# Kernel tuning notes

Hardware: AMD Instinct MI355X
Metric: run time of the kernel (lower is better)

## Reference

```python
import jax, jax.numpy as jnp
import numpy as np

D = 1024
H = 16
DH = D // H  # 64


def setup_inputs() -> dict:
    key = jax.random.key(0)
    ks = jax.random.split(key, 7)
    X = jax.random.normal(ks[0], (2, 2048, D), dtype=jnp.float32)
    # Per-head projection weights stacked along head axis: [H, D, DH]
    s = 1.0 / np.sqrt(D)
    Wq = jax.random.uniform(ks[1], (H, D, DH), jnp.float32, -s, s)
    Wk = jax.random.uniform(ks[2], (H, D, DH), jnp.float32, -s, s)
    Wv = jax.random.uniform(ks[3], (H, D, DH), jnp.float32, -s, s)
    bq = jax.random.uniform(ks[4], (H, DH), jnp.float32, -s, s)
    bk = jax.random.uniform(ks[5], (H, DH), jnp.float32, -s, s)
    bv = jax.random.uniform(ks[6], (H, DH), jnp.float32, -s, s)
    return {"X": X, "Wq": Wq, "bq": bq, "Wk": Wk, "bk": bk, "Wv": Wv, "bv": bv}


def reference(X, Wq, bq, Wk, bk, Wv, bv):
    B, S, _ = X.shape
    # Per-head linear projections (batched over heads): [B, H, S, DH]
    Q = jnp.einsum('bsd,hde->bhse', X, Wq) + bq[None, :, None, :]
    K = jnp.einsum('bsd,hde->bhse', X, Wk) + bk[None, :, None, :]
    V = jnp.einsum('bsd,hde->bhse', X, Wv) + bv[None, :, None, :]
    scale = jnp.sqrt(jnp.asarray(DH, dtype=X.dtype))
    QK = jnp.einsum('bhse,bhte->bhst', Q, K) / scale  # [B, H, S, S]
    # Faithful to source: softmax over full row FIRST, then lower-tri mask
    # (post-softmax tril, no renormalization).
    sQK = jax.nn.softmax(QK, axis=-1)
    tril = jnp.tril(jnp.ones((S, S), dtype=X.dtype))
    sQK = sQK * tril
    out = jnp.einsum('bhst,bhte->bhse', sQK, V)  # [B, H, S, DH]
    # Concatenate heads along feature dim (torch.cat over per-head outputs)
    return out.transpose(0, 2, 1, 3).reshape(B, S, H * DH)
```

## Files before the change

### kernel.cpp

```cpp
#include <hip/hip_runtime.h>
#include <math.h>

#define B_  2
#define S_  2048
#define D_  1024
#define H_  16
#define DH_ 64

typedef unsigned short u16;
typedef unsigned int   u32;
typedef _Float16       f16;
typedef _Float16 half8  __attribute__((ext_vector_type(8)));
typedef _Float16 half4  __attribute__((ext_vector_type(4)));
typedef float    f32x4  __attribute__((ext_vector_type(4)));

#if __has_builtin(__builtin_amdgcn_exp2f)
#define EXP2(x) __builtin_amdgcn_exp2f(x)
#else
#define EXP2(x) exp2f(x)
#endif

__device__ __forceinline__ u16 h_bits(f16 h){ return __builtin_bit_cast(u16, h); }

__device__ __forceinline__ void split8(float4 a, float4 b, uint4& H, uint4& L){
    float fv[8] = {a.x, a.y, a.z, a.w, b.x, b.y, b.z, b.w};
    u32 hw[4], lw[4];
    #pragma unroll
    for (int j = 0; j < 4; ++j){
        f16 h0 = (f16)fv[2*j],   h1 = (f16)fv[2*j+1];
        f16 l0 = (f16)(fv[2*j]   - (float)h0);
        f16 l1 = (f16)(fv[2*j+1] - (float)h1);
        hw[j] = h_bits(h0) | ((u32)h_bits(h1) << 16);
        lw[j] = h_bits(l0) | ((u32)h_bits(l1) << 16);
    }
    H = (uint4){hw[0], hw[1], hw[2], hw[3]};
    L = (uint4){lw[0], lw[1], lw[2], lw[3]};
}

__global__ __launch_bounds__(256) void prep_kernel(
    const float* __restrict__ Wq, const float* __restrict__ Wk,
    const float* __restrict__ Wv, u16* __restrict__ Wt)
{
    __shared__ float Wf[64][65];
    const int wb = blockIdx.x;
    const int c  = threadIdx.x;
    const int d0 = (wb & 15) * 64;
    const int h  = (wb >> 4) & 15;
    const int which = wb >> 8;
    const float* src = (which == 0) ? Wq : (which == 1) ? Wk : Wv;
    src += (size_t)h * D_ * DH_;

    #pragma unroll
    for (int it = 0; it < 4; ++it){
        int d  = (c >> 4) + 16 * it;
        int e4 = (c & 15) * 4;
        float4 v = *(const float4*)(src + (size_t)(d0 + d) * DH_ + e4);
        Wf[d][e4+0] = v.x; Wf[d][e4+1] = v.y; Wf[d][e4+2] = v.z; Wf[d][e4+3] = v.w;
    }
    __syncthreads();
    u16* dst = Wt + (size_t)(which * H_ + h) * DH_ * D_;
    #pragma unroll
    for (int it = 0; it < 4; ++it){
        int e  = (c >> 4) + 16 * it;
        int d4 = (c & 15) * 4;
        u16 q[4];
        #pragma unroll
        for (int j = 0; j < 4; ++j)
            q[j] = h_bits((f16)(Wf[d4 + j][e] * 64.0f));
        u32* p = (u32*)(dst + (size_t)e * D_ + d0 + d4);
        p[0] = q[0] | ((u32)q[1] << 16);
        p[1] = q[2] | ((u32)q[3] << 16);
    }
}

#define PKS 40

__global__ __launch_bounds__(256, 3) void proj_kernel(
    const float* __restrict__ X,
    const u16* __restrict__ Wt,
    const float* __restrict__ bq, const float* __restrict__ bk,
    const float* __restrict__ bv,
    f16* __restrict__ Qh, f16* __restrict__ Kh, f16* __restrict__ Vt)
{
    __shared__ u16 XsHi[128 * PKS], XsLo[128 * PKS], Bs[128 * PKS];

    const int tid  = threadIdx.x;
    const int lane = tid & 63;
    const int w    = tid >> 6;
    const int quad = lane >> 4;
    const int ln   = lane & 15;
    const int wr   = (w >> 1) * 64;
    const int wc   = (w & 1) * 64;
    const int m0   = blockIdx.x * 128;
    const int c0   = blockIdx.y * 128;

    const int sr  = tid >> 2;
    const int sch = (tid & 3) * 8;

    const float* x0 = X + (size_t)(m0 + sr) * D_ + sch;
    const float* x1 = x0 + (size_t)64 * D_;
    const u16*  wb0 = Wt + (size_t)(c0 + sr) * D_ + sch;
    const u16*  wb1 = wb0 + (size_t)64 * D_;

    float4 p00 = *(const float4*)x0, p01 = *(const float4*)(x0 + 4);
    float4 p10 = *(const float4*)x1, p11 = *(const float4*)(x1 + 4);
    uint4 rw0 = *(const uint4*)wb0, rw1 = *(const uint4*)wb1;
    uint4 h0, l0, h1, l1;
    split8(p00, p01, h0, l0);
    split8(p10, p11, h1, l1);

    f32x4 acc[4][4];
    #pragma unroll
    for (int i = 0; i < 4; ++i)
        #pragma unroll
        for (int j = 0; j < 4; ++j)
            acc[i][j] = (f32x4){0.f, 0.f, 0.f, 0.f};

    for (int k0 = 0; k0 < D_; k0 += 32){
        __syncthreads();
        *(uint4*)&XsHi[sr * PKS + sch]        = h0;
        *(uint4*)&XsHi[(sr + 64) * PKS + sch] = h1;
        *(uint4*)&XsLo[sr * PKS + sch]        = l0;
        *(uint4*)&XsLo[(sr + 64) * PKS + sch] = l1;
        *(uint4*)&Bs[sr * PKS + sch]          = rw0;
        *(uint4*)&Bs[(sr + 64) * PKS + sch]   = rw1;
        const int kn = k0 + 32;
        if (kn < D_){
            p00 = *(const float4*)(x0 + kn); p01 = *(const float4*)(x0 + kn + 4);
            p10 = *(const float4*)(x1 + kn); p11 = *(const float4*)(x1 + kn + 4);
            rw0 = *(const uint4*)(wb0 + kn); rw1 = *(const uint4*)(wb1 + kn);
        }
        __syncthreads();

        half8 ahi[4], alo[4], bf[4];
        #pragma unroll
        for (int mt = 0; mt < 4; ++mt){
            int row = wr + 16 * mt + ln;
            ahi[mt] = __builtin_bit_cast(half8, *(const uint4*)&XsHi[row * PKS + quad * 8]);
            alo[mt] = __builtin_bit_cast(half8, *(const uint4*)&XsLo[row * PKS + quad * 8]);
        }
        #pragma unroll
        for (int nt = 0; nt < 4; ++nt)
            bf[nt] = __builtin_bit_cast(half8,
                *(const uint4*)&Bs[(wc + 16 * nt + ln) * PKS + quad * 8]);
        #pragma unroll
        for (int mt = 0; mt < 4; ++mt)
            #pragma unroll
            for (int nt = 0; nt < 4; ++nt){
                acc[mt][nt] = __builtin_amdgcn_mfma_f32_16x16x32_f16(ahi[mt], bf[nt], acc[mt][nt], 0, 0, 0);
                acc[mt][nt] = __builtin_amdgcn_mfma_f32_16x16x32_f16(alo[mt], bf[nt], acc[mt][nt], 0, 0, 0);
            }

        if (kn < D_){
            split8(p00, p01, h0, l0);
            split8(p10, p11, h1, l1);
        }
    }

    const float QSCALE = 0.125f * 1.44269504088896340736f;
    const float INV64  = 0.015625f;
    #pragma unroll
    for (int nt = 0; nt < 4; ++nt){
        int colg  = c0 + wc + 16 * nt + ln;
        int which = colg >> 10;
        int h     = (colg >> 6) & 15;
        int e     = colg & 63;
        const float* bp = (which == 0) ? bq : (which == 1) ? bk : bv;
        float bias = bp[h * DH_ + e];
        if (which < 2){
            f16* op = (which == 0) ? Qh : Kh;
            float scale = (which == 0) ? QSCALE : 1.0f;
            #pragma unroll
            for (int mt = 0; mt < 4; ++mt)
                #pragma unroll
                for (int r = 0; r < 4; ++r){
                    int sg = m0 + wr + 16 * mt + 4 * quad + r;
                    int b  = sg >> 11;
                    int s  = sg & (S_ - 1);
                    float val = (acc[mt][nt][r] * INV64 + bias) * scale;
                    op[((size_t)(b * H_ + h) * S_ + s) * DH_ + e] = (f16)val;
                }
        } else {
            #pragma unroll
            for (int mt = 0; mt < 4; ++mt){
                int sg0 = m0 + wr + 16 * mt + 4 * quad;
                int b   = sg0 >> 11;
                int s0  = sg0 & (S_ - 1);
                u16 p[4];
                #pragma unroll
                for (int r = 0; r < 4; ++r)
                    p[r] = h_bits((f16)(acc[mt][nt][r] * INV64 + bias));
                uint2 pk;
                pk.x = p[0] | ((u32)p[1] << 16);
                pk.y = p[2] | ((u32)p[3] << 16);
                *(uint2*)((u16*)Vt + ((size_t)((b * H_ + h) * DH_ + e)) * S_ + s0) = pk;
            }
        }
    }
}

#define AKS 72
#define VKS 136

__global__ __launch_bounds__(256, 4) void attn_kernel(
    const f16* __restrict__ Qh, const f16* __restrict__ Kh,
    const f16* __restrict__ Vt, float* __restrict__ Out)
{
    __shared__ u16 Ks[128 * AKS];
    __shared__ u16 Vs[64 * VKS];

    const int tid  = threadIdx.x;
    const int lane = tid & 63;
    const int w    = tid >> 6;
    const int quad = lane >> 4;
    const int ln   = lane & 15;
    const int hb   = blockIdx.x;
    const int i    = blockIdx.y;
    const int h    = hb & 15;
    const int b    = hb >> 4;
    const int bh   = hb;
    const int sub  = w & 1;
    const int qbase = (w >> 1) ? (S_ - 32 * (i + 1) + 16 * sub)
                               : (32 * i + 16 * sub);
    const int vmax  = S_ - 32 * i - 1;

    const u16* Qg = (const u16*)Qh + (size_t)bh * S_ * DH_;
    const u16* Kg = (const u16*)Kh + (size_t)bh * S_ * DH_;
    const u16* Vg = (const u16*)Vt + (size_t)bh * DH_ * S_;

    half8 qf[2];
    #pragma unroll
    for (int ks = 0; ks < 2; ++ks)
        qf[ks] = __builtin_bit_cast(half8,
            *(const uint4*)(Qg + (size_t)(qbase + ln) * DH_ + 32 * ks + 8 * quad));

    const int kr = tid >> 3;
    const int kc = (tid & 7) * 8;

    uint4 ka = *(const uint4*)(Kg + (size_t)(kr)      * DH_ + kc);
    uint4 kb = *(const uint4*)(Kg + (size_t)(kr + 32) * DH_ + kc);
    uint4 kcg= *(const uint4*)(Kg + (size_t)(kr + 64) * DH_ + kc);
    uint4 kd = *(const uint4*)(Kg + (size_t)(kr + 96) * DH_ + kc);
    uint4 va = *(const uint4*)(Vg + (size_t)(kr)      * S_ + kc);
    uint4 vb = *(const uint4*)(Vg + (size_t)(kr + 32) * S_ + kc);
    uint4 vc = *(const uint4*)(Vg + (size_t)(kr)      * S_ + 64 + kc);
    uint4 vd = *(const uint4*)(Vg + (size_t)(kr + 32) * S_ + 64 + kc);

    float l_r = 0.f;
    f32x4 o_acc[4];
    #pragma unroll
    for (int nt = 0; nt < 4; ++nt) o_acc[nt] = (f32x4){0.f, 0.f, 0.f, 0.f};

    const int qrow   = qbase + ln;
    const int pv_lim = qbase + 15;

    for (int t0 = 0; t0 < S_; t0 += 128){
        __syncthreads();
        *(uint4*)&Ks[(kr)      * AKS + kc] = ka;
        *(uint4*)&Ks[(kr + 32) * AKS + kc] = kb;
        *(uint4*)&Ks[(kr + 64) * AKS + kc] = kcg;
        *(uint4*)&Ks[(kr + 96) * AKS + kc] = kd;
        if (t0 <= vmax){
            *(uint4*)&Vs[(kr)      * VKS + kc] = va;
            *(uint4*)&Vs[(kr + 32) * VKS + kc] = vb;
        }
        if (t0 + 64 <= vmax){
            *(uint4*)&Vs[(kr)      * VKS + 64 + kc] = vc;
            *(uint4*)&Vs[(kr + 32) * VKS + 64 + kc] = vd;
        }
        const int tp = t0 + 128;
        if (tp < S_){
            ka = *(const uint4*)(Kg + (size_t)(tp + kr)      * DH_ + kc);
            kb = *(const uint4*)(Kg + (size_t)(tp + kr + 32) * DH_ + kc);
            kcg= *(const uint4*)(Kg + (size_t)(tp + kr + 64) * DH_ + kc);
            kd = *(const uint4*)(Kg + (size_t)(tp + kr + 96) * DH_ + kc);
            if (tp <= vmax){
                va = *(const uint4*)(Vg + (size_t)(kr)      * S_ + tp + kc);
                vb = *(const uint4*)(Vg + (size_t)(kr + 32) * S_ + tp + kc);
            }
            if (tp + 64 <= vmax){
                vc = *(const uint4*)(Vg + (size_t)(kr)      * S_ + tp + 64 + kc);
                vd = *(const uint4*)(Vg + (size_t)(kr + 32) * S_ + tp + 64 + kc);
            }
        }
        __syncthreads();

        #pragma unroll
        for (int si = 0; si < 2; ++si){
            const int tb   = t0 + 64 * si;
            const int koff = 64 * si * AKS;
            const int voff = 64 * si;

            f32x4 sc[4];
            #pragma unroll
            for (int mt = 0; mt < 4; ++mt) sc[mt] = (f32x4){0.f, 0.f, 0.f, 0.f};
            #pragma unroll
            for (int ks = 0; ks < 2; ++ks)
                #pragma unroll
                for (int mt = 0; mt < 4; ++mt){
                    half8 kf = __builtin_bit_cast(half8,
                        *(const uint4*)&Ks[koff + (16 * mt + ln) * AKS + 32 * ks + 8 * quad]);
                    sc[mt] = __builtin_amdgcn_mfma_f32_16x16x32_f16(kf, qf[ks], sc[mt], 0, 0, 0);
                }

            #pragma unroll
            for (int mt = 0; mt < 4; ++mt)
                #pragma unroll
                for (int r = 0; r < 4; ++r)
                    sc[mt][r] = EXP2(sc[mt][r]);
            float s = ((sc[0][0] + sc[0][1] + sc[0][2] + sc[0][3]) +
                       (sc[1][0] + sc[1][1] + sc[1][2] + sc[1][3])) +
                      ((sc[2][0] + sc[2][1] + sc[2][2] + sc[2][3]) +
                       (sc[3][0] + sc[3][1] + sc[3][2] + sc[3][3]));
            s += __shfl_xor(s, 16);
            s += __shfl_xor(s, 32);
            l_r += s;

            #pragma unroll
            for (int mt = 0; mt < 4; ++mt){
                const int ts = tb + 16 * mt;
                if (ts <= pv_lim){
                    half4 pf;
                    if (ts == qbase){
                        int tq = ts + 4 * quad;
                        #pragma unroll
                        for (int r = 0; r < 4; ++r)
                            pf[r] = (tq + r > qrow) ? (f16)0.f : (f16)sc[mt][r];
                    } else {
                        #pragma unroll
                        for (int r = 0; r < 4; ++r)
                            pf[r] = (f16)sc[mt][r];
                    }
                    #pragma unroll
                    for (int nt = 0; nt < 4; ++nt){
                        half4 vf = __builtin_bit_cast(half4,
                            *(const uint2*)&Vs[(16 * nt + ln) * VKS + voff + 16 * mt + 4 * quad]);
                        o_acc[nt] = __builtin_amdgcn_mfma_f32_16x16x16f16(pf, vf, o_acc[nt], 0, 0, 0);
                    }
                }
            }
        }
    }

    #pragma unroll
    for (int r = 0; r < 4; ++r){
        float lv  = __shfl(l_r, (lane & 48) | (4 * quad + r));
        float inv = 1.0f / lv;
        int sg = qbase + 4 * quad + r;
        float* op = Out + ((size_t)b * S_ + sg) * D_ + h * DH_;
        #pragma unroll
        for (int nt = 0; nt < 4; ++nt)
            op[16 * nt + ln] = o_acc[nt][r] * inv;
    }
}

extern "C" void kernel_launch(void* const* d_in, const int* in_sizes, int n_in,
                              void* d_out, int out_size, void* d_ws, size_t ws_size,
                              hipStream_t stream)
{
    const float* X  = (const float*)d_in[0];
    const float* Wq = (const float*)d_in[1];
    const float* bq = (const float*)d_in[2];
    const float* Wk = (const float*)d_in[3];
    const float* bk = (const float*)d_in[4];
    const float* Wv = (const float*)d_in[5];
    const float* bv = (const float*)d_in[6];
    float* out = (float*)d_out;

    u16* Wt  = (u16*)d_ws;
    f16* Qh  = (f16*)(Wt + 3145728);
    f16* Kh  = Qh + 4194304;
    f16* Vt  = Kh + 4194304;

    prep_kernel<<<dim3(768), 256, 0, stream>>>(Wq, Wk, Wv, Wt);
    proj_kernel<<<dim3(32, 24), 256, 0, stream>>>(X, Wt, bq, bk, bv, Qh, Kh, Vt);
    attn_kernel<<<dim3(32, 32), 256, 0, stream>>>(Qh, Kh, Vt, out);
}
```

Before: 190.9 us.

## Fuse weight transpose and fp16 conversion into projection GEMM loads

Removes the separate prep kernel that transposed and converted the fp32 weights to fp16, and instead has the projection kernel read fp32 weights directly, convert them in registers and write them to shared memory in transposed form. This saves one launch and the round trip of the converted weight buffer through global memory. In exchange, the weight reads are now strided by 64 floats per element with coalescing only across 128 columns, the conversion is repeated in every M-block (32 times), and register pressure rises from holding 16 extra floats per thread.

```diff
diff --git a/kernel.cpp b/kernel.cpp
--- a/kernel.cpp
+++ b/kernel.cpp
@@ -37,47 +37,12 @@
     L = (uint4){lw[0], lw[1], lw[2], lw[3]};
 }
 
-__global__ __launch_bounds__(256) void prep_kernel(
-    const float* __restrict__ Wq, const float* __restrict__ Wk,
-    const float* __restrict__ Wv, u16* __restrict__ Wt)
-{
-    __shared__ float Wf[64][65];
-    const int wb = blockIdx.x;
-    const int c  = threadIdx.x;
-    const int d0 = (wb & 15) * 64;
-    const int h  = (wb >> 4) & 15;
-    const int which = wb >> 8;
-    const float* src = (which == 0) ? Wq : (which == 1) ? Wk : Wv;
-    src += (size_t)h * D_ * DH_;
-
-    #pragma unroll
-    for (int it = 0; it < 4; ++it){
-        int d  = (c >> 4) + 16 * it;
-        int e4 = (c & 15) * 4;
-        float4 v = *(const float4*)(src + (size_t)(d0 + d) * DH_ + e4);
-        Wf[d][e4+0] = v.x; Wf[d][e4+1] = v.y; Wf[d][e4+2] = v.z; Wf[d][e4+3] = v.w;
-    }
-    __syncthreads();
-    u16* dst = Wt + (size_t)(which * H_ + h) * DH_ * D_;
-    #pragma unroll
-    for (int it = 0; it < 4; ++it){
-        int e  = (c >> 4) + 16 * it;
-        int d4 = (c & 15) * 4;
-        u16 q[4];
-        #pragma unroll
-        for (int j = 0; j < 4; ++j)
-            q[j] = h_bits((f16)(Wf[d4 + j][e] * 64.0f));
-        u32* p = (u32*)(dst + (size_t)e * D_ + d0 + d4);
-        p[0] = q[0] | ((u32)q[1] << 16);
-        p[1] = q[2] | ((u32)q[3] << 16);
-    }
-}
-
 #define PKS 40
 
 __global__ __launch_bounds__(256, 3) void proj_kernel(
     const float* __restrict__ X,
-    const u16* __restrict__ Wt,
+    const float* __restrict__ Wq, const float* __restrict__ Wk,
+    const float* __restrict__ Wv,
     const float* __restrict__ bq, const float* __restrict__ bk,
     const float* __restrict__ bv,
     f16* __restrict__ Qh, f16* __restrict__ Kh, f16* __restrict__ Vt)
@@ -96,18 +61,39 @@
 
     const int sr  = tid >> 2;
     const int sch = (tid & 3) * 8;
-
     const float* x0 = X + (size_t)(m0 + sr) * D_ + sch;
     const float* x1 = x0 + (size_t)64 * D_;
-    const u16*  wb0 = Wt + (size_t)(c0 + sr) * D_ + sch;
-    const u16*  wb1 = wb0 + (size_t)64 * D_;
+
+    const int eg = tid & 127;
+    const int dg = tid >> 7;
+    const int colg0  = c0 + eg;
+    const int whichE = colg0 >> 10;
+    const int hE     = (colg0 >> 6) & 15;
+    const float* wbase = ((whichE == 0) ? Wq : (whichE == 1) ? Wk : Wv)
+                         + (size_t)hE * D_ * DH_ + (colg0 & 63);
 
     float4 p00 = *(const float4*)x0, p01 = *(const float4*)(x0 + 4);
     float4 p10 = *(const float4*)x1, p11 = *(const float4*)(x1 + 4);
-    uint4 rw0 = *(const uint4*)wb0, rw1 = *(const uint4*)wb1;
     uint4 h0, l0, h1, l1;
     split8(p00, p01, h0, l0);
     split8(p10, p11, h1, l1);
+
+    float wv_[16];
+    #pragma unroll
+    for (int i = 0; i < 16; ++i)
+        wv_[i] = wbase[(size_t)(dg * 16 + i) * 64];
+    uint4 wq0, wq1;
+    {
+        u32 bw[8];
+        #pragma unroll
+        for (int j = 0; j < 8; ++j){
+            u16 a = h_bits((f16)(wv_[2*j]   * 64.0f));
+            u16 b = h_bits((f16)(wv_[2*j+1] * 64.0f));
+            bw[j] = a | ((u32)b << 16);
+        }
+        wq0 = (uint4){bw[0], bw[1], bw[2], bw[3]};
+        wq1 = (uint4){bw[4], bw[5], bw[6], bw[7]};
+    }
 
     f32x4 acc[4][4];
     #pragma unroll
@@ -122,13 +108,15 @@
         *(uint4*)&XsHi[(sr + 64) * PKS + sch] = h1;
         *(uint4*)&XsLo[sr * PKS + sch]        = l0;
         *(uint4*)&XsLo[(sr + 64) * PKS + sch] = l1;
-        *(uint4*)&Bs[sr * PKS + sch]          = rw0;
-        *(uint4*)&Bs[(sr + 64) * PKS + sch]   = rw1;
+        *(uint4*)&Bs[eg * PKS + dg * 16]      = wq0;
+        *(uint4*)&Bs[eg * PKS + dg * 16 + 8]  = wq1;
         const int kn = k0 + 32;
         if (kn < D_){
             p00 = *(const float4*)(x0 + kn); p01 = *(const float4*)(x0 + kn + 4);
             p10 = *(const float4*)(x1 + kn); p11 = *(const float4*)(x1 + kn + 4);
-            rw0 = *(const uint4*)(wb0 + kn); rw1 = *(const uint4*)(wb1 + kn);
+            #pragma unroll
+            for (int i = 0; i < 16; ++i)
+                wv_[i] = wbase[(size_t)(kn + dg * 16 + i) * 64];
         }
         __syncthreads();
 
@@ -154,6 +142,15 @@
         if (kn < D_){
             split8(p00, p01, h0, l0);
             split8(p10, p11, h1, l1);
+            u32 bw[8];
+            #pragma unroll
+            for (int j = 0; j < 8; ++j){
+                u16 a = h_bits((f16)(wv_[2*j]   * 64.0f));
+                u16 b = h_bits((f16)(wv_[2*j+1] * 64.0f));
+                bw[j] = a | ((u32)b << 16);
+            }
+            wq0 = (uint4){bw[0], bw[1], bw[2], bw[3]};
+            wq1 = (uint4){bw[4], bw[5], bw[6], bw[7]};
         }
     }
 
@@ -367,12 +364,10 @@
     const float* bv = (const float*)d_in[6];
     float* out = (float*)d_out;
 
-    u16* Wt  = (u16*)d_ws;
-    f16* Qh  = (f16*)(Wt + 3145728);
+    f16* Qh  = (f16*)d_ws;
     f16* Kh  = Qh + 4194304;
     f16* Vt  = Kh + 4194304;
 
-    prep_kernel<<<dim3(768), 256, 0, stream>>>(Wq, Wk, Wv, Wt);
-    proj_kernel<<<dim3(32, 24), 256, 0, stream>>>(X, Wt, bq, bk, bv, Qh, Kh, Vt);
+    proj_kernel<<<dim3(32, 24), 256, 0, stream>>>(X, Wq, Wk, Wv, bq, bk, bv, Qh, Kh, Vt);
     attn_kernel<<<dim3(32, 32), 256, 0, stream>>>(Qh, Kh, Vt, out);
 }
```

Result: slower. 198.3 us (+3.9%).
